# Performance work log

Hardware: AMD Instinct MI355X
Metric: run time of the kernel (lower is better)

Reference implementation:

```python
import jax, jax.numpy as jnp
import numpy as np

A, B, D, H = 64, 256, 128, 512  # seq rows, columns (encoder batch / decode loop), n_dims, hidden


def _lstm_step(Wih, Whh, bih, bhh, h, c, x):
    # x: [N, D], h/c: [N, H]; PyTorch gate order i, f, g, o
    gates = x @ Wih.T + bih + h @ Whh.T + bhh  # [N, 4H]
    i, f, g, o = jnp.split(gates, 4, axis=-1)
    c = jax.nn.sigmoid(f) * c + jax.nn.sigmoid(i) * jnp.tanh(g)
    h = jax.nn.sigmoid(o) * jnp.tanh(c)
    return h, c


def setup_inputs() -> dict:
    key = jax.random.key(0)
    ks = jax.random.split(key, 12)
    s = 0.05
    inp = {
        "input_tensor": jax.random.normal(ks[0], (A, B, D), jnp.float32),
        "enc_Wih": jax.random.normal(ks[1], (4 * H, D), jnp.float32) * s,
        "enc_Whh": jax.random.normal(ks[2], (4 * H, H), jnp.float32) * s,
        "enc_bih": jax.random.normal(ks[3], (4 * H,), jnp.float32) * s,
        "enc_bhh": jax.random.normal(ks[4], (4 * H,), jnp.float32) * s,
        "dec_Wih": jax.random.normal(ks[5], (4 * H, D), jnp.float32) * s,
        "dec_Whh": jax.random.normal(ks[6], (4 * H, H), jnp.float32) * s,
        "dec_bih": jax.random.normal(ks[7], (4 * H,), jnp.float32) * s,
        "dec_bhh": jax.random.normal(ks[8], (4 * H,), jnp.float32) * s,
        "lin_W": jax.random.normal(ks[9], (D, H), jnp.float32) * s,
        "lin_b": jax.random.normal(ks[10], (D,), jnp.float32) * s,
    }
    return inp


def reference(input_tensor, enc_Wih, enc_Whh, enc_bih, enc_bhh,
              dec_Wih, dec_Whh, dec_bih, dec_bhh, lin_W, lin_b):
    a, b, d = input_tensor.shape
    h_dim = enc_Whh.shape[1]
    dt = input_tensor.dtype

    # ---- encoder: seq-first LSTM over dim0 (len a), batch = b ----
    def e_step(hc, x_t):
        h, c = hc
        h, c = _lstm_step(enc_Wih, enc_Whh, enc_bih, enc_bhh, h, c, x_t)
        return (h, c), None

    h0 = jnp.zeros((b, h_dim), dt)
    (hN, cN), _ = jax.lax.scan(e_step, (h0, h0), input_tensor)
    # hidden[0][:, -1].unsqueeze(1): keep only the LAST batch element -> [1, H]
    dh, dc = hN[-1:], cN[-1:]

    # ---- decoder: loop i = b-1 .. 0; emit linear(h) then run length-a LSTM on column i ----
    def col_step(hc, x_col):  # x_col: [a, d]
        h, c = hc
        out_i = (h @ lin_W.T + lin_b)[0]  # [d], emitted BEFORE processing the column

        def t_step(hc2, x_t):
            h2, c2 = hc2
            h2, c2 = _lstm_step(dec_Wih, dec_Whh, dec_bih, dec_bhh, h2, c2, x_t[None])
            return (h2, c2), None

        (h, c), _ = jax.lax.scan(t_step, (h, c), x_col)
        return (h, c), out_i

    x_cols = jnp.flip(jnp.transpose(input_tensor, (1, 0, 2)), 0)  # [b, a, d], reversed i
    _, outs = jax.lax.scan(col_step, (dh, dc), x_cols)  # [b, d] in reversed order
    outs = jnp.flip(outs, 0)
    # outputs[:, i, :] = [1, d] row broadcast across all a rows
    return jnp.broadcast_to(outs[None, :, :], (a, b, d))
```

## Files before the change

### kernel.cpp

```cpp
#include <hip/hip_runtime.h>
#include <math.h>

#define A_ 64
#define B_ 256
#define D_ 128
#define H_ 512
#define STOT 16384
#define NWG 32

#define XCC_GETREG_IMM (20 | (31 << 11))

#define OFF_XT    0
#define N_XT      (A_*D_*B_)
#define OFF_HT0   (OFF_XT + N_XT)
#define OFF_HT1   (OFF_HT0 + H_*B_)
#define OFF_CT    (OFF_HT1 + H_*B_)
#define OFF_HTAP  (OFF_CT + H_*B_)
#define OFF_HB64  (OFF_HTAP + B_*H_)
#define OFF_CINIT (OFF_HB64 + 4*H_)
#define OFF_ELECT (OFF_CINIT + H_)

__device__ __forceinline__ float sigf(float x) {
  return __builtin_amdgcn_rcpf(1.0f + __expf(-x));
}
__device__ __forceinline__ float tanhfast(float x) {
  return 1.0f - 2.0f * __builtin_amdgcn_rcpf(__expf(2.0f * x) + 1.0f);
}

__device__ __forceinline__ unsigned long long load_nt(const unsigned long long* p) {
  unsigned long long v;
  asm volatile("global_load_dwordx2 %0, %1, off nt\n\ts_waitcnt vmcnt(0)"
               : "=&v"(v) : "v"(p) : "memory");
  return v;
}
__device__ __forceinline__ unsigned long long load_inv(const unsigned long long* p) {
  unsigned long long v;
  asm volatile("buffer_inv sc0\n\t"
               "global_load_dwordx2 %0, %1, off nt\n\ts_waitcnt vmcnt(0)"
               : "=&v"(v) : "v"(p) : "memory");
  return v;
}
__device__ __forceinline__ void store_nt(unsigned long long* p, unsigned long long v) {
  asm volatile("global_store_dwordx2 %0, %1, off nt" :: "v"(p), "v"(v) : "memory");
}

__global__ void init1(const float* __restrict__ in0, float* __restrict__ ws) {
  float* XT  = ws + OFF_XT;
  float* HT0 = ws + OFF_HT0;
  float* CT  = ws + OFF_CT;
  int stride = gridDim.x * blockDim.x;
  for (int idx = blockIdx.x * blockDim.x + threadIdx.x; idx < N_XT; idx += stride) {
    int t = idx >> 15;
    int k = (idx >> 8) & 127;
    int b = idx & 255;
    XT[idx] = in0[t * (B_ * D_) + b * D_ + k];
    if (idx < H_ * B_) { HT0[idx] = 0.f; CT[idx] = 0.f; }
  }
}

__global__ __launch_bounds__(256) void enc_step(
    const float* __restrict__ XT, const float* __restrict__ Wih,
    const float* __restrict__ Whh, const float* __restrict__ bih,
    const float* __restrict__ bhh, const float* __restrict__ Hin,
    float* __restrict__ Hout, float* __restrict__ C, int t) {
  __shared__ float Wt[16 * 68];
  __shared__ float XHt[16 * 32];
  __shared__ float gs[64 * 33];
  const int tid = threadIdx.x;
  const int jt = blockIdx.x;
  const int bt = blockIdx.y;
  const int rr = tid >> 4;
  const int bb = tid & 15;

  float acc[4][2];
#pragma unroll
  for (int i = 0; i < 4; ++i) {
    int r = 4 * rr + i;
    int Row = ((r >> 4) << 9) + (jt << 4) + (r & 15);
    float bv = bih[Row] + bhh[Row];
    acc[i][0] = bv; acc[i][1] = bv;
  }

  for (int kt = 0; kt < 40; ++kt) {
    int k0 = kt << 4;
    __syncthreads();
#pragma unroll
    for (int e = 0; e < 4; ++e) {
      int idx = tid + (e << 8);
      int kk = idx & 15, r = idx >> 4;
      int Row = ((r >> 4) << 9) + (jt << 4) + (r & 15);
      int k = k0 + kk;
      float v = (k < D_) ? Wih[Row * D_ + k] : Whh[Row * H_ + (k - D_)];
      Wt[kk * 68 + r] = v;
    }
#pragma unroll
    for (int e = 0; e < 2; ++e) {
      int idx = tid + (e << 8);
      int kk = idx >> 5, b = idx & 31;
      int k = k0 + kk;
      int gb = (bt << 5) + b;
      float v = (k < D_) ? XT[(t * D_ + k) * B_ + gb] : Hin[(k - D_) * B_ + gb];
      XHt[kk * 32 + b] = v;
    }
    __syncthreads();
#pragma unroll
    for (int kk = 0; kk < 16; ++kk) {
      const float4 wv = *(const float4*)&Wt[kk * 68 + 4 * rr];
      const float2 xv = *(const float2*)&XHt[kk * 32 + 2 * bb];
      acc[0][0] += wv.x * xv.x; acc[0][1] += wv.x * xv.y;
      acc[1][0] += wv.y * xv.x; acc[1][1] += wv.y * xv.y;
      acc[2][0] += wv.z * xv.x; acc[2][1] += wv.z * xv.y;
      acc[3][0] += wv.w * xv.x; acc[3][1] += wv.w * xv.y;
    }
  }
  __syncthreads();
#pragma unroll
  for (int i = 0; i < 4; ++i) {
    gs[(4 * rr + i) * 33 + 2 * bb]     = acc[i][0];
    gs[(4 * rr + i) * 33 + 2 * bb + 1] = acc[i][1];
  }
  __syncthreads();
#pragma unroll
  for (int e = 0; e < 2; ++e) {
    int idx = tid + (e << 8);
    int jj = idx >> 5, b = idx & 31;
    int gb = (bt << 5) + b;
    float iv = gs[jj * 33 + b];
    float fv = gs[(16 + jj) * 33 + b];
    float gv = gs[(32 + jj) * 33 + b];
    float ov = gs[(48 + jj) * 33 + b];
    int addr = ((jt << 4) + jj) * B_ + gb;
    float c = C[addr];
    c = sigf(fv) * c + sigf(iv) * tanhf(gv);
    C[addr] = c;
    Hout[addr] = sigf(ov) * tanhf(c);
  }
}

__global__ void init2(float* __restrict__ ws) {
  const float* Hfin = ws + OFF_HT0;
  const float* CT   = ws + OFF_CT;
  unsigned long long* HB = (unsigned long long*)(ws + OFF_HB64);
  float* CIN  = ws + OFF_CINIT;
  float* HTAP = ws + OFF_HTAP;
  int* EL     = (int*)(ws + OFF_ELECT);
  int j = threadIdx.x;
  float hj = Hfin[j * B_ + 255];
  HB[H_ + j] = (unsigned long long)__float_as_uint(hj);
  HB[j]      = 0xFFFFFFFF00000000ull;
  CIN[j]  = CT[j * B_ + 255];
  HTAP[j] = hj;
  if (j < 8) EL[j] = 0;
  if (j == 8) EL[8] = -1;
}

__global__ __launch_bounds__(1024) void decoder(
    const float* __restrict__ in0, const float* __restrict__ Wih,
    const float* __restrict__ Whh, const float* __restrict__ bih,
    const float* __restrict__ bhh, float* __restrict__ ws) {
  unsigned long long* HB = (unsigned long long*)(ws + OFF_HB64);
  float* HTAP = ws + OFF_HTAP;
  const float* CIN = ws + OFF_CINIT;

  __shared__ float part[2][16 * 64];
  __shared__ float hstage[H_];
  __shared__ int role;

  const int tid = threadIdx.x;

  if (tid == 0) {
    unsigned xcc = ((unsigned)__builtin_amdgcn_s_getreg(XCC_GETREG_IMM)) & 7u;
    int* EL = (int*)(ws + OFF_ELECT);
    int r = __hip_atomic_fetch_add(&EL[xcc], 1, __ATOMIC_RELAXED,
                                   __HIP_MEMORY_SCOPE_AGENT);
    int myrole = -1;
    if (r < NWG) {
      if (r == NWG - 1) {
        int exp = -1;
        __hip_atomic_compare_exchange_strong(&EL[8], &exp, (int)xcc,
            __ATOMIC_RELAXED, __ATOMIC_RELAXED, __HIP_MEMORY_SCOPE_AGENT);
      }
      int wx;
      do {
        wx = __hip_atomic_load(&EL[8], __ATOMIC_RELAXED, __HIP_MEMORY_SCOPE_AGENT);
        if (wx == -1) __builtin_amdgcn_s_sleep(2);
      } while (wx == -1);
      if (wx == (int)xcc) myrole = r;
    }
    role = myrole;
  }
  __syncthreads();
  if (role < 0) return;
  const int w = role;

  const int v = tid >> 6;
  const int l = tid & 63;
  const int R = ((l >> 4) << 9) + (w << 4) + (l & 15);

  float4 wa[8];
#pragma unroll
  for (int k = 0; k < 8; ++k)
    wa[k] = *(const float4*)&Whh[R * H_ + (v << 5) + 4 * k];
  float4 wx0 = *(const float4*)&Wih[R * D_ + (v << 3)];
  float4 wx1 = *(const float4*)&Wih[R * D_ + (v << 3) + 4];

  float bias = 0.f, c = 0.f;
  if (v == 0) {
    bias = bih[R] + bhh[R];
    if (l < 16) c = CIN[(w << 4) + l];
  }

  const int pe = (v << 5) + (l & 31);

  for (int s = 0; s < STOT; ++s) {
    const int tt = s & 63;
    const int bc = 255 - (s >> 6);
    const float* xp = in0 + (tt * B_ + bc) * D_ + (v << 3);
    float4 x0 = *(const float4*)xp;
    float4 x1 = *(const float4*)(xp + 4);

    unsigned long long* slot = &HB[(((s + 1) & 1) << 9) + pe];
    unsigned long long pk;
    int spins = 0;
    for (;;) {
      pk = ((++spins & 63) == 0) ? load_inv(slot) : load_nt(slot);
      if (__all((unsigned)(pk >> 32) == (unsigned)s)) break;
    }
    if (l < 32) hstage[pe] = __uint_as_float((unsigned)pk);

    float p = wx0.x * x0.x + wx0.y * x0.y + wx0.z * x0.z + wx0.w * x0.w
            + wx1.x * x1.x + wx1.y * x1.y + wx1.z * x1.z + wx1.w * x1.w;

    const float4* hp = (const float4*)&hstage[v << 5];
#pragma unroll
    for (int k = 0; k < 8; ++k) {
      float4 h4 = hp[k];
      p += wa[k].x * h4.x + wa[k].y * h4.y + wa[k].z * h4.z + wa[k].w * h4.w;
    }
    part[s & 1][(v << 6) + l] = p;
    __syncthreads();

    if (v == 0) {
      float g = bias;
#pragma unroll
      for (int j = 0; j < 16; ++j) g += part[s & 1][(j << 6) + l];
      const int e = l & 15;
      float vi = __shfl(g, e);
      float vf = __shfl(g, e + 16);
      float vg = __shfl(g, e + 32);
      float vo = __shfl(g, e + 48);
      if (l < 16) {
        c = sigf(vf) * c + sigf(vi) * tanhfast(vg);
        float hn = sigf(vo) * tanhfast(c);
        if ((s & 63) == 63) {
          int q = (s >> 6) + 1;
          if (q < 256) HTAP[q * H_ + (w << 4) + l] = hn;
        }
        unsigned long long opk =
            ((unsigned long long)(unsigned)(s + 1) << 32) | __float_as_uint(hn);
        store_nt(&HB[((s & 1) << 9) + (w << 4) + l], opk);
      }
    }
  }
}

__global__ __launch_bounds__(128) void out_proj(
    const float* __restrict__ ws, const float* __restrict__ linW,
    const float* __restrict__ linb, float* __restrict__ out) {
  const float* HTAP = ws + OFF_HTAP;
  __shared__ float hs[H_];
  const int b = blockIdx.x;
  const int i = 255 - b;
  const int d = threadIdx.x;
  *(float4*)&hs[4 * d] = *(const float4*)&HTAP[i * H_ + 4 * d];
  __syncthreads();
  float acc = linb[d];
#pragma unroll 8
  for (int k = 0; k < H_; k += 4) {
    float4 w4 = *(const float4*)&linW[d * H_ + k];
    acc += w4.x * hs[k] + w4.y * hs[k + 1] + w4.z * hs[k + 2] + w4.w * hs[k + 3];
  }
  for (int a = 0; a < A_; ++a)
    out[(a * B_ + b) * D_ + d] = acc;
}

extern "C" void kernel_launch(void* const* d_in, const int* in_sizes, int n_in,
                              void* d_out, int out_size, void* d_ws, size_t ws_size,
                              hipStream_t stream) {
  const float* in0  = (const float*)d_in[0];
  const float* eWih = (const float*)d_in[1];
  const float* eWhh = (const float*)d_in[2];
  const float* ebih = (const float*)d_in[3];
  const float* ebhh = (const float*)d_in[4];
  const float* dWih = (const float*)d_in[5];
  const float* dWhh = (const float*)d_in[6];
  const float* dbih = (const float*)d_in[7];
  const float* dbhh = (const float*)d_in[8];
  const float* linW = (const float*)d_in[9];
  const float* linb = (const float*)d_in[10];
  float* ws = (float*)d_ws;
  float* out = (float*)d_out;

  init1<<<2048, 256, 0, stream>>>(in0, ws);

  const float* XT = ws + OFF_XT;
  for (int t = 0; t < 64; ++t) {
    float* Hin  = ws + ((t & 1) ? OFF_HT1 : OFF_HT0);
    float* Hout = ws + ((t & 1) ? OFF_HT0 : OFF_HT1);
    enc_step<<<dim3(32, 8), 256, 0, stream>>>(XT, eWih, eWhh, ebih, ebhh,
                                              Hin, Hout, ws + OFF_CT, t);
  }
  init2<<<1, 512, 0, stream>>>(ws);
  decoder<<<256, 1024, 0, stream>>>(in0, dWih, dWhh, dbih, dbhh, ws);
  out_proj<<<256, 128, 0, stream>>>(ws, linW, linb, out);
}
```

Before: 22.33 ms.

## Replace per-element tagged h broadcast with per-workgroup flags and LDS relay

Each hidden value used to carry its own step tag in a 64-bit packed word, and every wave polled all 512 entries itself. Now h values are stored as plain floats, and each workgroup publishes a single step counter after its stores drain. Only wave 0 polls the 32 flags and relays readiness to the other waves through an LDS variable; the gate-combining role moves to wave 15. This cuts global polling traffic, but it adds a store-then-flag ordering dependency, an extra vmcnt wait, an LDS spin, and a possible memory-visibility race if the flag is seen before the data.

```diff
diff --git a/kernel.cpp b/kernel.cpp
--- a/kernel.cpp
+++ b/kernel.cpp
@@ -16,8 +16,9 @@
 #define OFF_HT1   (OFF_HT0 + H_*B_)
 #define OFF_CT    (OFF_HT1 + H_*B_)
 #define OFF_HTAP  (OFF_CT + H_*B_)
-#define OFF_HB64  (OFF_HTAP + B_*H_)
-#define OFF_CINIT (OFF_HB64 + 4*H_)
+#define OFF_HB    (OFF_HTAP + B_*H_)
+#define OFF_FLG   (OFF_HB + 2*H_)
+#define OFF_CINIT (OFF_FLG + 32)
 #define OFF_ELECT (OFF_CINIT + H_)
 
 __device__ __forceinline__ float sigf(float x) {
@@ -27,21 +28,21 @@
   return 1.0f - 2.0f * __builtin_amdgcn_rcpf(__expf(2.0f * x) + 1.0f);
 }
 
-__device__ __forceinline__ unsigned long long load_nt(const unsigned long long* p) {
-  unsigned long long v;
-  asm volatile("global_load_dwordx2 %0, %1, off nt\n\ts_waitcnt vmcnt(0)"
+__device__ __forceinline__ unsigned load_nt32(const unsigned* p) {
+  unsigned v;
+  asm volatile("global_load_dword %0, %1, off nt\n\ts_waitcnt vmcnt(0)"
                : "=&v"(v) : "v"(p) : "memory");
   return v;
 }
-__device__ __forceinline__ unsigned long long load_inv(const unsigned long long* p) {
-  unsigned long long v;
+__device__ __forceinline__ unsigned load_inv32(const unsigned* p) {
+  unsigned v;
   asm volatile("buffer_inv sc0\n\t"
-               "global_load_dwordx2 %0, %1, off nt\n\ts_waitcnt vmcnt(0)"
+               "global_load_dword %0, %1, off nt\n\ts_waitcnt vmcnt(0)"
                : "=&v"(v) : "v"(p) : "memory");
   return v;
 }
-__device__ __forceinline__ void store_nt(unsigned long long* p, unsigned long long v) {
-  asm volatile("global_store_dwordx2 %0, %1, off nt" :: "v"(p), "v"(v) : "memory");
+__device__ __forceinline__ void store_nt32(unsigned* p, unsigned v) {
+  asm volatile("global_store_dword %0, %1, off nt" :: "v"(p), "v"(v) : "memory");
 }
 
 __global__ void init1(const float* __restrict__ in0, float* __restrict__ ws) {
@@ -140,16 +141,18 @@
 __global__ void init2(float* __restrict__ ws) {
   const float* Hfin = ws + OFF_HT0;
   const float* CT   = ws + OFF_CT;
-  unsigned long long* HB = (unsigned long long*)(ws + OFF_HB64);
+  float* HB   = ws + OFF_HB;
+  unsigned* FLG = (unsigned*)(ws + OFF_FLG);
   float* CIN  = ws + OFF_CINIT;
   float* HTAP = ws + OFF_HTAP;
   int* EL     = (int*)(ws + OFF_ELECT);
   int j = threadIdx.x;
   float hj = Hfin[j * B_ + 255];
-  HB[H_ + j] = (unsigned long long)__float_as_uint(hj);
-  HB[j]      = 0xFFFFFFFF00000000ull;
+  HB[H_ + j] = hj;
+  HB[j]      = 0.f;
   CIN[j]  = CT[j * B_ + 255];
   HTAP[j] = hj;
+  if (j < 32) FLG[j] = 0;
   if (j < 8) EL[j] = 0;
   if (j == 8) EL[8] = -1;
 }
@@ -158,12 +161,14 @@
     const float* __restrict__ in0, const float* __restrict__ Wih,
     const float* __restrict__ Whh, const float* __restrict__ bih,
     const float* __restrict__ bhh, float* __restrict__ ws) {
-  unsigned long long* HB = (unsigned long long*)(ws + OFF_HB64);
+  float* HB = ws + OFF_HB;
+  unsigned* FLG = (unsigned*)(ws + OFF_FLG);
   float* HTAP = ws + OFF_HTAP;
   const float* CIN = ws + OFF_CINIT;
 
   __shared__ float part[2][16 * 64];
   __shared__ float hstage[H_];
+  __shared__ int lflag;
   __shared__ int role;
 
   const int tid = threadIdx.x;
@@ -188,6 +193,7 @@
       if (wx == (int)xcc) myrole = r;
     }
     role = myrole;
+    lflag = -1;
   }
   __syncthreads();
   if (role < 0) return;
@@ -205,7 +211,7 @@
   float4 wx1 = *(const float4*)&Wih[R * D_ + (v << 3) + 4];
 
   float bias = 0.f, c = 0.f;
-  if (v == 0) {
+  if (v == 15) {
     bias = bih[R] + bhh[R];
     if (l < 16) c = CIN[(w << 4) + l];
   }
@@ -213,34 +219,42 @@
   const int pe = (v << 5) + (l & 31);
 
   for (int s = 0; s < STOT; ++s) {
+    const int p = (s + 1) & 1;
     const int tt = s & 63;
     const int bc = 255 - (s >> 6);
     const float* xp = in0 + (tt * B_ + bc) * D_ + (v << 3);
     float4 x0 = *(const float4*)xp;
     float4 x1 = *(const float4*)(xp + 4);
 
-    unsigned long long* slot = &HB[(((s + 1) & 1) << 9) + pe];
-    unsigned long long pk;
-    int spins = 0;
-    for (;;) {
-      pk = ((++spins & 63) == 0) ? load_inv(slot) : load_nt(slot);
-      if (__all((unsigned)(pk >> 32) == (unsigned)s)) break;
-    }
-    if (l < 32) hstage[pe] = __uint_as_float((unsigned)pk);
-
-    float p = wx0.x * x0.x + wx0.y * x0.y + wx0.z * x0.z + wx0.w * x0.w
-            + wx1.x * x1.x + wx1.y * x1.y + wx1.z * x1.z + wx1.w * x1.w;
+    if (v == 0) {
+      const unsigned* fp = FLG + (l & 31);
+      int spins = 0;
+      for (;;) {
+        unsigned f = ((++spins & 63) == 0) ? load_inv32(fp) : load_nt32(fp);
+        if (__all((int)f >= s)) break;
+      }
+      if (l == 0) *(volatile int*)&lflag = s;
+    } else {
+      while (*(volatile int*)&lflag < s) { }
+      __asm__ volatile("" ::: "memory");
+    }
+
+    if (l < 32)
+      hstage[pe] = __uint_as_float(load_nt32((const unsigned*)&HB[(p << 9) + pe]));
+
+    float pacc = wx0.x * x0.x + wx0.y * x0.y + wx0.z * x0.z + wx0.w * x0.w
+               + wx1.x * x1.x + wx1.y * x1.y + wx1.z * x1.z + wx1.w * x1.w;
 
     const float4* hp = (const float4*)&hstage[v << 5];
 #pragma unroll
     for (int k = 0; k < 8; ++k) {
       float4 h4 = hp[k];
-      p += wa[k].x * h4.x + wa[k].y * h4.y + wa[k].z * h4.z + wa[k].w * h4.w;
-    }
-    part[s & 1][(v << 6) + l] = p;
+      pacc += wa[k].x * h4.x + wa[k].y * h4.y + wa[k].z * h4.z + wa[k].w * h4.w;
+    }
+    part[s & 1][(v << 6) + l] = pacc;
     __syncthreads();
 
-    if (v == 0) {
+    if (v == 15) {
       float g = bias;
 #pragma unroll
       for (int j = 0; j < 16; ++j) g += part[s & 1][(j << 6) + l];
@@ -256,10 +270,11 @@
           int q = (s >> 6) + 1;
           if (q < 256) HTAP[q * H_ + (w << 4) + l] = hn;
         }
-        unsigned long long opk =
-            ((unsigned long long)(unsigned)(s + 1) << 32) | __float_as_uint(hn);
-        store_nt(&HB[((s & 1) << 9) + (w << 4) + l], opk);
+        store_nt32((unsigned*)&HB[((s & 1) << 9) + (w << 4) + l],
+                   __float_as_uint(hn));
+        asm volatile("s_waitcnt vmcnt(0)" ::: "memory");
       }
+      if (l == 0) store_nt32(&FLG[w], (unsigned)(s + 1));
     }
   }
 }
```

New measurement: 26.39 ms. +18.2%, slower.
